# Performance work log

Hardware: AMD Instinct MI355X
Metric: run time of the kernel (lower is better)

Reference implementation:

```python
import jax, jax.numpy as jnp
import numpy as np

SCENE_BOUND = 1.5

def _trilinear_sample(vol, g):
    """torch.nn.functional.grid_sample (3D, bilinear, zeros padding, align_corners=True).

    vol: (C, D, H, W) volume.
    g:   (N, 3) normalized coords in [-1, 1], ordered (x, y, z) where
         x indexes W, y indexes H, z indexes D (torch convention).
    returns: (N, C) interpolated features.
    """
    C, D, H, W = vol.shape
    sizes = jnp.array([W, H, D], dtype=g.dtype)
    pix = (g + 1.0) * 0.5 * (sizes - 1.0)  # align_corners=True mapping
    x, y, z = pix[:, 0], pix[:, 1], pix[:, 2]
    x0f, y0f, z0f = jnp.floor(x), jnp.floor(y), jnp.floor(z)
    fx, fy, fz = x - x0f, y - y0f, z - z0f
    x0, y0, z0 = x0f.astype(jnp.int32), y0f.astype(jnp.int32), z0f.astype(jnp.int32)
    vol_flat = vol.reshape(C, -1)  # (C, D*H*W)
    out = jnp.zeros((g.shape[0], C), dtype=vol.dtype)
    for dz in (0, 1):
        for dy in (0, 1):
            for dx in (0, 1):
                xi, yi, zi = x0 + dx, y0 + dy, z0 + dz
                w = ((fx if dx else 1.0 - fx)
                     * (fy if dy else 1.0 - fy)
                     * (fz if dz else 1.0 - fz))
                inb = ((xi >= 0) & (xi < W) & (yi >= 0) & (yi < H)
                       & (zi >= 0) & (zi < D))
                xi_c = jnp.clip(xi, 0, W - 1)
                yi_c = jnp.clip(yi, 0, H - 1)
                zi_c = jnp.clip(zi, 0, D - 1)
                flat = (zi_c * H + yi_c) * W + xi_c  # (N,)
                feat = jnp.take(vol_flat, flat, axis=1)  # (C, N)
                out = out + (w * inb.astype(w.dtype))[:, None] * feat.T
    return out


def setup_inputs() -> dict:
    key = jax.random.key(0)
    k1, k2, k3, k4, k5 = jax.random.split(key, 5)
    N, R = 2_000_000, 128
    xyz = (jax.random.uniform(k1, (N, 3), dtype=jnp.float32) * 2.0 - 1.0) * (SCENE_BOUND * 0.99)
    base_density = jax.random.normal(k2, (1, 1, R, R, R), dtype=jnp.float32)
    base_sh = jax.random.normal(k3, (1, 27, R, R, R), dtype=jnp.float32)
    detail_density = jax.random.normal(k4, (1, 1, R, R, R), dtype=jnp.float32) * 0.1
    detail_sh = jax.random.normal(k5, (1, 27, R, R, R), dtype=jnp.float32) * 0.1
    return {"xyz": xyz, "base_density": base_density, "base_sh": base_sh,
            "detail_density": detail_density, "detail_sh": detail_sh}


def reference(xyz, base_density, base_sh, detail_density, detail_sh):
    # grid property: concat(base_density + detail_density, base_sh + detail_sh)
    vol = jnp.concatenate([base_density + detail_density,
                           base_sh + detail_sh], axis=1)[0]  # (C, R, R, R)
    g = xyz / SCENE_BOUND  # normalized to [-1, 1]
    return _trilinear_sample(vol, g)  # (N, C), matches query()'s permuted output
```

## Files before the change

kernel.cpp:

```cpp
#include <hip/hip_runtime.h>
#include <hip/hip_fp16.h>
#include <cstdint>
#include <cstddef>

#define RR     128
#define VV     (RR * RR * RR)
#define NCH    28
#define CPAD   32
#define NCD    16
#define NCELLS 4096
#define REG    9
#define RV     (REG * REG * REG)
#define CAPMAX 768
#define CAPMIN 576
#define OVFCAP 262144

__device__ __forceinline__ unsigned short f2h(float f) {
    __half h = __float2half(f);
    return *reinterpret_cast<unsigned short*>(&h);
}
__device__ __forceinline__ float2 up2(unsigned int u) {
    __half2 h = *reinterpret_cast<__half2*>(&u);
    return __half22float2(h);
}

__device__ __forceinline__ void point_coords(float x, float y, float z,
                                             float& px, float& py, float& pz,
                                             int& ix, int& iy, int& iz) {
    const float S = 63.5f / 1.5f;
    px = fmaf(x, S, 63.5f);
    py = fmaf(y, S, 63.5f);
    pz = fmaf(z, S, 63.5f);
    ix = min(max((int)floorf(px), 0), RR - 2);
    iy = min(max((int)floorf(py), 0), RR - 2);
    iz = min(max((int)floorf(pz), 0), RR - 2);
}

__device__ __forceinline__ void presum_body(
    int tid,
    const float* __restrict__ bden, const float* __restrict__ bsh,
    const float* __restrict__ dden, const float* __restrict__ dsh,
    unsigned short* __restrict__ ws)
{
    if (tid >= VV) return;
    unsigned short s[CPAD];
    s[0] = f2h(bden[tid] + dden[tid]);
#pragma unroll
    for (int c = 1; c < NCH; ++c) {
        size_t off = (size_t)(c - 1) * VV + tid;
        s[c] = f2h(bsh[off] + dsh[off]);
    }
#pragma unroll
    for (int c = NCH; c < CPAD; ++c) s[c] = 0;

    uint4* w = (uint4*)(ws + (size_t)tid * CPAD);
#pragma unroll
    for (int q = 0; q < 4; ++q) {
        uint4 v;
        v.x = (unsigned int)s[q*8+0] | ((unsigned int)s[q*8+1] << 16);
        v.y = (unsigned int)s[q*8+2] | ((unsigned int)s[q*8+3] << 16);
        v.z = (unsigned int)s[q*8+4] | ((unsigned int)s[q*8+5] << 16);
        v.w = (unsigned int)s[q*8+6] | ((unsigned int)s[q*8+7] << 16);
        w[q] = v;
    }
}

__global__ __launch_bounds__(256) void presum_scatter(
    const float* __restrict__ bden, const float* __restrict__ bsh,
    const float* __restrict__ dden, const float* __restrict__ dsh,
    const float* __restrict__ xyz, int N, int CAP,
    unsigned short* __restrict__ vol, float4* __restrict__ sorted,
    unsigned int* __restrict__ cur, unsigned int* __restrict__ ovf,
    unsigned int* __restrict__ ovfcnt, int presumBlocks)
{
    int b = blockIdx.x;
    if (b < presumBlocks) {
        presum_body(b * 256 + threadIdx.x, bden, bsh, dden, dsh, vol);
        return;
    }
    int n = (b - presumBlocks) * 256 + threadIdx.x;
    if (n >= N) return;
    const float* xp = xyz + (size_t)n * 3;
    float px, py, pz; int ix, iy, iz;
    point_coords(xp[0], xp[1], xp[2], px, py, pz, ix, iy, iz);
    int cell = ((iz >> 3) * NCD + (iy >> 3)) * NCD + (ix >> 3);
    unsigned int slot = atomicAdd(&cur[cell], 1u);
    if (slot < (unsigned int)CAP) {
        sorted[(size_t)cell * CAP + slot] = make_float4(px, py, pz, __int_as_float(n));
    } else {
        unsigned int o = atomicAdd(ovfcnt, 1u);
        if (o < (unsigned int)OVFCAP) ovf[o] = n;
    }
}

__global__ __launch_bounds__(512) void cell_gather(
    const unsigned short* __restrict__ vol,
    const float4* __restrict__ sorted, const unsigned int* __restrict__ cur,
    int CAP, float* __restrict__ out)
{
    __shared__ uint4 lds16[RV * 4];

    int bid = blockIdx.x;
    int cid = (bid & 7) * (NCELLS / 8) + (bid >> 3);
    int cx = cid & 15, cy = (cid >> 4) & 15, cz = cid >> 8;
    int x0 = cx << 3, y0 = cy << 3, z0 = cz << 3;

    for (int i = threadIdx.x; i < RV * 4; i += 512) {
        int v = i >> 2, j = i & 3;
        int rz = v / 81, rem = v - rz * 81;
        int ry = rem / 9, rx = rem - ry * 9;
        int zg = min(z0 + rz, RR - 1);
        int yg = min(y0 + ry, RR - 1);
        int xg = min(x0 + rx, RR - 1);
        const uint4* src = (const uint4*)(vol + (size_t)((zg * RR + yg) * RR + xg) * CPAD);
        lds16[v * 4 + (j ^ (v & 3))] = src[j];
    }
    __syncthreads();

    int cnt = (int)min(cur[cid], (unsigned int)CAP);
    const float4* sp = sorted + (size_t)cid * CAP;
    int g = threadIdx.x >> 2, t = threadIdx.x & 3;

    for (int p = g; p < cnt; p += 128) {
        float4 pt = sp[p];
        float px = pt.x, py = pt.y, pz = pt.z;
        int idx = __float_as_int(pt.w);

        float fx0 = floorf(px), fy0 = floorf(py), fz0 = floorf(pz);
        float fx = px - fx0, fy = py - fy0, fz = pz - fz0;
        int lx = min(max((int)fx0, 0), RR - 2) - x0;
        int ly = min(max((int)fy0, 0), RR - 2) - y0;
        int lz = min(max((int)fz0, 0), RR - 2) - z0;

        float wx[2] = {1.0f - fx, fx};
        float wy[2] = {1.0f - fy, fy};
        float wz[2] = {1.0f - fz, fz};

        float acc[8];
#pragma unroll
        for (int k = 0; k < 8; ++k) acc[k] = 0.0f;

#pragma unroll
        for (int dz = 0; dz < 2; ++dz)
#pragma unroll
        for (int dy = 0; dy < 2; ++dy)
#pragma unroll
        for (int dx = 0; dx < 2; ++dx) {
            int v = ((lz + dz) * 9 + (ly + dy)) * 9 + (lx + dx);
            float w = wz[dz] * wy[dy] * wx[dx];
            const uint4 q = lds16[v * 4 + (t ^ (v & 3))];
            float2 p0 = up2(q.x), p1 = up2(q.y), p2 = up2(q.z), p3 = up2(q.w);
            acc[0] = fmaf(w, p0.x, acc[0]);
            acc[1] = fmaf(w, p0.y, acc[1]);
            acc[2] = fmaf(w, p1.x, acc[2]);
            acc[3] = fmaf(w, p1.y, acc[3]);
            acc[4] = fmaf(w, p2.x, acc[4]);
            acc[5] = fmaf(w, p2.y, acc[5]);
            acc[6] = fmaf(w, p3.x, acc[6]);
            acc[7] = fmaf(w, p3.y, acc[7]);
        }

        float* op = out + (size_t)idx * NCH + t * 8;
        if (t < 3) {
            *(float4*)op       = make_float4(acc[0], acc[1], acc[2], acc[3]);
            *(float4*)(op + 4) = make_float4(acc[4], acc[5], acc[6], acc[7]);
        } else {
            *(float4*)op = make_float4(acc[0], acc[1], acc[2], acc[3]);
        }
    }
}

__global__ __launch_bounds__(256) void tail_gather(
    const float* __restrict__ xyz, const unsigned short* __restrict__ vol,
    const unsigned int* __restrict__ ovf, const unsigned int* __restrict__ ovfcnt,
    float* __restrict__ out)
{
    int m = (int)min(*ovfcnt, (unsigned int)OVFCAP);
    for (int i = blockIdx.x * 256 + threadIdx.x; i < m; i += gridDim.x * 256) {
        int n = (int)ovf[i];
        const float* xp = xyz + (size_t)n * 3;
        float px, py, pz; int ix, iy, iz;
        point_coords(xp[0], xp[1], xp[2], px, py, pz, ix, iy, iz);
        float fx = px - floorf(px), fy = py - floorf(py), fz = pz - floorf(pz);
        float wx[2] = {1.0f - fx, fx}, wy[2] = {1.0f - fy, fy}, wz[2] = {1.0f - fz, fz};
        int ibase = (iz * RR + iy) * RR + ix;
        for (int t = 0; t < 4; ++t) {
            float acc[8];
#pragma unroll
            for (int k = 0; k < 8; ++k) acc[k] = 0.0f;
#pragma unroll
            for (int dz = 0; dz < 2; ++dz)
#pragma unroll
            for (int dy = 0; dy < 2; ++dy)
#pragma unroll
            for (int dx = 0; dx < 2; ++dx) {
                int vidx = ibase + dz * (RR * RR) + dy * RR + dx;
                float w = wz[dz] * wy[dy] * wx[dx];
                const uint4 q = *(const uint4*)((const char*)vol + (size_t)vidx * (CPAD * 2) + t * 16);
                float2 p0 = up2(q.x), p1 = up2(q.y), p2 = up2(q.z), p3 = up2(q.w);
                acc[0] = fmaf(w, p0.x, acc[0]);
                acc[1] = fmaf(w, p0.y, acc[1]);
                acc[2] = fmaf(w, p1.x, acc[2]);
                acc[3] = fmaf(w, p1.y, acc[3]);
                acc[4] = fmaf(w, p2.x, acc[4]);
                acc[5] = fmaf(w, p2.y, acc[5]);
                acc[6] = fmaf(w, p3.x, acc[6]);
                acc[7] = fmaf(w, p3.y, acc[7]);
            }
            float* op = out + (size_t)n * NCH + t * 8;
            if (t < 3) {
                *(float4*)op       = make_float4(acc[0], acc[1], acc[2], acc[3]);
                *(float4*)(op + 4) = make_float4(acc[4], acc[5], acc[6], acc[7]);
            } else {
                *(float4*)op = make_float4(acc[0], acc[1], acc[2], acc[3]);
            }
        }
    }
}

__global__ __launch_bounds__(256) void presum_kernel(
    const float* __restrict__ bden, const float* __restrict__ bsh,
    const float* __restrict__ dden, const float* __restrict__ dsh,
    unsigned short* __restrict__ ws)
{
    presum_body(blockIdx.x * 256 + threadIdx.x, bden, bsh, dden, dsh, ws);
}

__global__ __launch_bounds__(256) void gather_kernel(
    const float* __restrict__ xyz,
    const unsigned short* __restrict__ vol,
    float* __restrict__ out, int N)
{
    int tid = blockIdx.x * 256 + threadIdx.x;
    int n = tid >> 2;
    int t = tid & 3;
    if (n >= N) return;

    const float* xp = xyz + (size_t)n * 3;
    float px, py, pz; int ix, iy, iz;
    point_coords(xp[0], xp[1], xp[2], px, py, pz, ix, iy, iz);
    float fx = px - floorf(px), fy = py - floorf(py), fz = pz - floorf(pz);
    float wx[2] = {1.0f - fx, fx}, wy[2] = {1.0f - fy, fy}, wz[2] = {1.0f - fz, fz};

    int ibase = (iz * RR + iy) * RR + ix;
    const char* basep = (const char*)vol + (size_t)t * 16;

    float acc[8];
#pragma unroll
    for (int k = 0; k < 8; ++k) acc[k] = 0.0f;

#pragma unroll
    for (int dz = 0; dz < 2; ++dz)
#pragma unroll
    for (int dy = 0; dy < 2; ++dy)
#pragma unroll
    for (int dx = 0; dx < 2; ++dx) {
        int vidx = ibase + dz * (RR * RR) + dy * RR + dx;
        float w = wz[dz] * wy[dy] * wx[dx];
        const uint4 q = *(const uint4*)(basep + (size_t)vidx * (CPAD * 2));
        float2 p0 = up2(q.x), p1 = up2(q.y), p2 = up2(q.z), p3 = up2(q.w);
        acc[0] = fmaf(w, p0.x, acc[0]);
        acc[1] = fmaf(w, p0.y, acc[1]);
        acc[2] = fmaf(w, p1.x, acc[2]);
        acc[3] = fmaf(w, p1.y, acc[3]);
        acc[4] = fmaf(w, p2.x, acc[4]);
        acc[5] = fmaf(w, p2.y, acc[5]);
        acc[6] = fmaf(w, p3.x, acc[6]);
        acc[7] = fmaf(w, p3.y, acc[7]);
    }

    float* op = out + (size_t)n * NCH + t * 8;
    if (t < 3) {
        *(float4*)op       = make_float4(acc[0], acc[1], acc[2], acc[3]);
        *(float4*)(op + 4) = make_float4(acc[4], acc[5], acc[6], acc[7]);
    } else {
        *(float4*)op = make_float4(acc[0], acc[1], acc[2], acc[3]);
    }
}

__global__ __launch_bounds__(256) void gather_fallback(
    const float* __restrict__ xyz,
    const float* __restrict__ bden, const float* __restrict__ bsh,
    const float* __restrict__ dden, const float* __restrict__ dsh,
    float* __restrict__ out, int N)
{
    int n = blockIdx.x * 256 + threadIdx.x;
    if (n >= N) return;
    const float* xp = xyz + (size_t)n * 3;
    float px, py, pz; int ix, iy, iz;
    point_coords(xp[0], xp[1], xp[2], px, py, pz, ix, iy, iz);
    float fx = px - floorf(px), fy = py - floorf(py), fz = pz - floorf(pz);
    float wx[2] = {1.0f - fx, fx}, wy[2] = {1.0f - fy, fy}, wz[2] = {1.0f - fz, fz};

    int idx[8]; float w[8];
#pragma unroll
    for (int k = 0; k < 8; ++k) {
        int dz = (k >> 2) & 1, dy = (k >> 1) & 1, dx = k & 1;
        idx[k] = ((iz + dz) * RR + (iy + dy)) * RR + (ix + dx);
        w[k] = wz[dz] * wy[dy] * wx[dx];
    }
#pragma unroll
    for (int c = 0; c < NCH; ++c) {
        const float* bp = (c == 0) ? bden : (bsh + (size_t)(c - 1) * VV);
        const float* dp = (c == 0) ? dden : (dsh + (size_t)(c - 1) * VV);
        float a = 0.0f;
#pragma unroll
        for (int k = 0; k < 8; ++k)
            a = fmaf(w[k], bp[idx[k]] + dp[idx[k]], a);
        out[(size_t)n * NCH + c] = a;
    }
}

extern "C" void kernel_launch(void* const* d_in, const int* in_sizes, int n_in,
                              void* d_out, int out_size, void* d_ws, size_t ws_size,
                              hipStream_t stream) {
    const float* xyz  = (const float*)d_in[0];
    const float* bden = (const float*)d_in[1];
    const float* bsh  = (const float*)d_in[2];
    const float* dden = (const float*)d_in[3];
    const float* dsh  = (const float*)d_in[4];
    float* out = (float*)d_out;
    int N = in_sizes[0] / 3;

    size_t volBytes = (size_t)VV * CPAD * sizeof(unsigned short);
    size_t ovfBytes = (size_t)OVFCAP * 4;
    size_t ctrBytes = (size_t)(NCELLS + 1) * 4;

    long long availForSorted = (long long)ws_size - (long long)(volBytes + ovfBytes + ctrBytes + 64);
    int CAP = 0;
    if (availForSorted > 0) {
        long long c = availForSorted / ((long long)NCELLS * 16);
        CAP = (int)(c > CAPMAX ? CAPMAX : c);
    }

    if (CAP >= CAPMIN) {
        char* w = (char*)d_ws;
        float4* sorted      = (float4*)w;
        size_t sortedBytes  = (size_t)NCELLS * CAP * 16;
        unsigned short* vol = (unsigned short*)(w + sortedBytes);
        unsigned int* ovf   = (unsigned int*)(w + sortedBytes + volBytes);
        unsigned int* cur   = (unsigned int*)(w + sortedBytes + volBytes + ovfBytes);
        unsigned int* ovfcnt = cur + NCELLS;

        hipMemsetAsync(cur, 0, (NCELLS + 1) * sizeof(unsigned int), stream);
        int presumBlocks  = (VV + 255) / 256;
        int scatterBlocks = (N + 255) / 256;
        presum_scatter<<<presumBlocks + scatterBlocks, 256, 0, stream>>>(
            bden, bsh, dden, dsh, xyz, N, CAP,
            vol, sorted, cur, ovf, ovfcnt, presumBlocks);
        cell_gather<<<NCELLS, 512, 0, stream>>>(vol, sorted, cur, CAP, out);
        tail_gather<<<32, 256, 0, stream>>>(xyz, vol, ovf, ovfcnt, out);
    } else if (ws_size >= volBytes) {
        presum_kernel<<<(VV + 255) / 256, 256, 0, stream>>>(
            bden, bsh, dden, dsh, (unsigned short*)d_ws);
        long long threads = (long long)N * 4;
        gather_kernel<<<(unsigned int)((threads + 255) / 256), 256, 0, stream>>>(
            xyz, (const unsigned short*)d_ws, out, N);
    } else {
        gather_fallback<<<(N + 255) / 256, 256, 0, stream>>>(
            xyz, bden, bsh, dden, dsh, out, N);
    }
}
```

Baseline: 799.3 us.

## Shard cell counters into sub-buckets, chunk volume layout, fuse tail gather

Spreads the scatter atomics over 8 sub-buckets per cell, chosen by block index, so fewer threads contend on the same counter. The gather block merges the sub-buckets through a small prefix sum. The packed fp16 volume is rearranged into 64-voxel chunks so the presum writes and the halo loads coalesce. The overflow tail pass is folded into extra blocks of the cell gather kernel, capacities are sized from the mean occupancy, and presum loads are batched with a higher occupancy launch bound. Costs are more bucket memory and a per-point sub-bucket lookup.

```diff
diff --git a/kernel.cpp b/kernel.cpp
--- a/kernel.cpp
+++ b/kernel.cpp
@@ -2,6 +2,7 @@
 #include <hip/hip_fp16.h>
 #include <cstdint>
 #include <cstddef>
+#include <cmath>
 
 #define RR     128
 #define VV     (RR * RR * RR)
@@ -9,11 +10,11 @@
 #define CPAD   32
 #define NCD    16
 #define NCELLS 4096
+#define NSUB   8
 #define REG    9
 #define RV     (REG * REG * REG)
-#define CAPMAX 768
-#define CAPMIN 576
-#define OVFCAP 262144
+#define OVFCAP (1 << 20)
+#define TAILB  32
 
 __device__ __forceinline__ unsigned short f2h(float f) {
     __half h = __float2half(f);
@@ -22,6 +23,10 @@
 __device__ __forceinline__ float2 up2(unsigned int u) {
     __half2 h = *reinterpret_cast<__half2*>(&u);
     return __half22float2(h);
+}
+
+__device__ __forceinline__ size_t chunk_at(int V, int q) {
+    return ((size_t)(V >> 6)) * 256 + (q << 6) + (V & 63);
 }
 
 __device__ __forceinline__ void point_coords(float x, float y, float z,
@@ -36,24 +41,43 @@
     iz = min(max((int)floorf(pz), 0), RR - 2);
 }
 
+__device__ __forceinline__ void corner_accum(
+    const uint4 q, float w, float* acc)
+{
+    float2 p0 = up2(q.x), p1 = up2(q.y), p2 = up2(q.z), p3 = up2(q.w);
+    acc[0] = fmaf(w, p0.x, acc[0]);
+    acc[1] = fmaf(w, p0.y, acc[1]);
+    acc[2] = fmaf(w, p1.x, acc[2]);
+    acc[3] = fmaf(w, p1.y, acc[3]);
+    acc[4] = fmaf(w, p2.x, acc[4]);
+    acc[5] = fmaf(w, p2.y, acc[5]);
+    acc[6] = fmaf(w, p3.x, acc[6]);
+    acc[7] = fmaf(w, p3.y, acc[7]);
+}
+
 __device__ __forceinline__ void presum_body(
     int tid,
     const float* __restrict__ bden, const float* __restrict__ bsh,
     const float* __restrict__ dden, const float* __restrict__ dsh,
-    unsigned short* __restrict__ ws)
+    unsigned short* __restrict__ vol)
 {
     if (tid >= VV) return;
+    float vb[27], vd[27];
+    float v0 = bden[tid] + dden[tid];
+#pragma unroll
+    for (int c = 0; c < 27; ++c) vb[c] = bsh[(size_t)c * VV + tid];
+#pragma unroll
+    for (int c = 0; c < 27; ++c) vd[c] = dsh[(size_t)c * VV + tid];
+
     unsigned short s[CPAD];
-    s[0] = f2h(bden[tid] + dden[tid]);
-#pragma unroll
-    for (int c = 1; c < NCH; ++c) {
-        size_t off = (size_t)(c - 1) * VV + tid;
-        s[c] = f2h(bsh[off] + dsh[off]);
-    }
+    s[0] = f2h(v0);
+#pragma unroll
+    for (int c = 0; c < 27; ++c) s[c + 1] = f2h(vb[c] + vd[c]);
 #pragma unroll
     for (int c = NCH; c < CPAD; ++c) s[c] = 0;
 
-    uint4* w = (uint4*)(ws + (size_t)tid * CPAD);
+    uint4* volq = (uint4*)vol;
+    int grp = tid >> 6, lane = tid & 63;
 #pragma unroll
     for (int q = 0; q < 4; ++q) {
         uint4 v;
@@ -61,14 +85,14 @@
         v.y = (unsigned int)s[q*8+2] | ((unsigned int)s[q*8+3] << 16);
         v.z = (unsigned int)s[q*8+4] | ((unsigned int)s[q*8+5] << 16);
         v.w = (unsigned int)s[q*8+6] | ((unsigned int)s[q*8+7] << 16);
-        w[q] = v;
-    }
-}
-
-__global__ __launch_bounds__(256) void presum_scatter(
+        volq[(size_t)grp * 256 + (q << 6) + lane] = v;
+    }
+}
+
+__global__ __launch_bounds__(256, 4) void presum_scatter(
     const float* __restrict__ bden, const float* __restrict__ bsh,
     const float* __restrict__ dden, const float* __restrict__ dsh,
-    const float* __restrict__ xyz, int N, int CAP,
+    const float* __restrict__ xyz, int N, int CAPS,
     unsigned short* __restrict__ vol, float4* __restrict__ sorted,
     unsigned int* __restrict__ cur, unsigned int* __restrict__ ovf,
     unsigned int* __restrict__ ovfcnt, int presumBlocks)
@@ -84,9 +108,11 @@
     float px, py, pz; int ix, iy, iz;
     point_coords(xp[0], xp[1], xp[2], px, py, pz, ix, iy, iz);
     int cell = ((iz >> 3) * NCD + (iy >> 3)) * NCD + (ix >> 3);
-    unsigned int slot = atomicAdd(&cur[cell], 1u);
-    if (slot < (unsigned int)CAP) {
-        sorted[(size_t)cell * CAP + slot] = make_float4(px, py, pz, __int_as_float(n));
+    int sub = b & 7;
+    unsigned int slot = atomicAdd(&cur[sub * NCELLS + cell], 1u);
+    if (slot < (unsigned int)CAPS) {
+        sorted[((size_t)sub * NCELLS + cell) * CAPS + slot] =
+            make_float4(px, py, pz, __int_as_float(n));
     } else {
         unsigned int o = atomicAdd(ovfcnt, 1u);
         if (o < (unsigned int)OVFCAP) ovf[o] = n;
@@ -94,35 +120,89 @@
 }
 
 __global__ __launch_bounds__(512) void cell_gather(
-    const unsigned short* __restrict__ vol,
+    const unsigned short* __restrict__ vol, const float* __restrict__ xyz,
     const float4* __restrict__ sorted, const unsigned int* __restrict__ cur,
-    int CAP, float* __restrict__ out)
-{
+    const unsigned int* __restrict__ ovf, const unsigned int* __restrict__ ovfcnt,
+    int CAPS, float* __restrict__ out)
+{
+    const uint4* vol4 = (const uint4*)vol;
+    int bid = blockIdx.x;
+
+    if (bid >= NCELLS) {
+        int m = (int)min(*ovfcnt, (unsigned int)OVFCAP);
+        for (int i = (bid - NCELLS) * 512 + threadIdx.x; i < m; i += TAILB * 512) {
+            int n = (int)ovf[i];
+            const float* xp = xyz + (size_t)n * 3;
+            float px, py, pz; int ix, iy, iz;
+            point_coords(xp[0], xp[1], xp[2], px, py, pz, ix, iy, iz);
+            float fx = px - floorf(px), fy = py - floorf(py), fz = pz - floorf(pz);
+            float wx[2] = {1.0f - fx, fx}, wy[2] = {1.0f - fy, fy}, wz[2] = {1.0f - fz, fz};
+            int ibase = (iz * RR + iy) * RR + ix;
+            for (int t = 0; t < 4; ++t) {
+                float acc[8];
+#pragma unroll
+                for (int k = 0; k < 8; ++k) acc[k] = 0.0f;
+#pragma unroll
+                for (int dz = 0; dz < 2; ++dz)
+#pragma unroll
+                for (int dy = 0; dy < 2; ++dy)
+#pragma unroll
+                for (int dx = 0; dx < 2; ++dx) {
+                    int vidx = ibase + dz * (RR * RR) + dy * RR + dx;
+                    float w = wz[dz] * wy[dy] * wx[dx];
+                    corner_accum(vol4[chunk_at(vidx, t)], w, acc);
+                }
+                float* op = out + (size_t)n * NCH + t * 8;
+                if (t < 3) {
+                    *(float4*)op       = make_float4(acc[0], acc[1], acc[2], acc[3]);
+                    *(float4*)(op + 4) = make_float4(acc[4], acc[5], acc[6], acc[7]);
+                } else {
+                    *(float4*)op = make_float4(acc[0], acc[1], acc[2], acc[3]);
+                }
+            }
+        }
+        return;
+    }
+
     __shared__ uint4 lds16[RV * 4];
-
-    int bid = blockIdx.x;
+    __shared__ unsigned int pref[NSUB + 1];
+
     int cid = (bid & 7) * (NCELLS / 8) + (bid >> 3);
     int cx = cid & 15, cy = (cid >> 4) & 15, cz = cid >> 8;
     int x0 = cx << 3, y0 = cy << 3, z0 = cz << 3;
 
-    for (int i = threadIdx.x; i < RV * 4; i += 512) {
-        int v = i >> 2, j = i & 3;
+    if (threadIdx.x == 0) {
+        unsigned int a = 0;
+        pref[0] = 0;
+#pragma unroll
+        for (int s = 0; s < NSUB; ++s) {
+            a += min(cur[s * NCELLS + cid], (unsigned int)CAPS);
+            pref[s + 1] = a;
+        }
+    }
+
+    for (int i = threadIdx.x; i < 4 * RV; i += 512) {
+        int q = i / RV;
+        int v = i - q * RV;
         int rz = v / 81, rem = v - rz * 81;
         int ry = rem / 9, rx = rem - ry * 9;
         int zg = min(z0 + rz, RR - 1);
         int yg = min(y0 + ry, RR - 1);
         int xg = min(x0 + rx, RR - 1);
-        const uint4* src = (const uint4*)(vol + (size_t)((zg * RR + yg) * RR + xg) * CPAD);
-        lds16[v * 4 + (j ^ (v & 3))] = src[j];
+        int V = (zg * RR + yg) * RR + xg;
+        lds16[v * 4 + (q ^ (v & 3))] = vol4[chunk_at(V, q)];
     }
     __syncthreads();
 
-    int cnt = (int)min(cur[cid], (unsigned int)CAP);
-    const float4* sp = sorted + (size_t)cid * CAP;
+    int total = (int)pref[NSUB];
     int g = threadIdx.x >> 2, t = threadIdx.x & 3;
 
-    for (int p = g; p < cnt; p += 128) {
-        float4 pt = sp[p];
+    for (int vp = g; vp < total; vp += 128) {
+        int s = 0;
+#pragma unroll
+        for (int k = 0; k < NSUB - 1; ++k) s += (vp >= (int)pref[k + 1]);
+        int p = vp - (int)pref[s];
+        float4 pt = sorted[((size_t)s * NCELLS + cid) * CAPS + p];
         float px = pt.x, py = pt.y, pz = pt.z;
         int idx = __float_as_int(pt.w);
 
@@ -148,16 +228,7 @@
         for (int dx = 0; dx < 2; ++dx) {
             int v = ((lz + dz) * 9 + (ly + dy)) * 9 + (lx + dx);
             float w = wz[dz] * wy[dy] * wx[dx];
-            const uint4 q = lds16[v * 4 + (t ^ (v & 3))];
-            float2 p0 = up2(q.x), p1 = up2(q.y), p2 = up2(q.z), p3 = up2(q.w);
-            acc[0] = fmaf(w, p0.x, acc[0]);
-            acc[1] = fmaf(w, p0.y, acc[1]);
-            acc[2] = fmaf(w, p1.x, acc[2]);
-            acc[3] = fmaf(w, p1.y, acc[3]);
-            acc[4] = fmaf(w, p2.x, acc[4]);
-            acc[5] = fmaf(w, p2.y, acc[5]);
-            acc[6] = fmaf(w, p3.x, acc[6]);
-            acc[7] = fmaf(w, p3.y, acc[7]);
+            corner_accum(lds16[v * 4 + (t ^ (v & 3))], w, acc);
         }
 
         float* op = out + (size_t)idx * NCH + t * 8;
@@ -170,60 +241,12 @@
     }
 }
 
-__global__ __launch_bounds__(256) void tail_gather(
-    const float* __restrict__ xyz, const unsigned short* __restrict__ vol,
-    const unsigned int* __restrict__ ovf, const unsigned int* __restrict__ ovfcnt,
-    float* __restrict__ out)
-{
-    int m = (int)min(*ovfcnt, (unsigned int)OVFCAP);
-    for (int i = blockIdx.x * 256 + threadIdx.x; i < m; i += gridDim.x * 256) {
-        int n = (int)ovf[i];
-        const float* xp = xyz + (size_t)n * 3;
-        float px, py, pz; int ix, iy, iz;
-        point_coords(xp[0], xp[1], xp[2], px, py, pz, ix, iy, iz);
-        float fx = px - floorf(px), fy = py - floorf(py), fz = pz - floorf(pz);
-        float wx[2] = {1.0f - fx, fx}, wy[2] = {1.0f - fy, fy}, wz[2] = {1.0f - fz, fz};
-        int ibase = (iz * RR + iy) * RR + ix;
-        for (int t = 0; t < 4; ++t) {
-            float acc[8];
-#pragma unroll
-            for (int k = 0; k < 8; ++k) acc[k] = 0.0f;
-#pragma unroll
-            for (int dz = 0; dz < 2; ++dz)
-#pragma unroll
-            for (int dy = 0; dy < 2; ++dy)
-#pragma unroll
-            for (int dx = 0; dx < 2; ++dx) {
-                int vidx = ibase + dz * (RR * RR) + dy * RR + dx;
-                float w = wz[dz] * wy[dy] * wx[dx];
-                const uint4 q = *(const uint4*)((const char*)vol + (size_t)vidx * (CPAD * 2) + t * 16);
-                float2 p0 = up2(q.x), p1 = up2(q.y), p2 = up2(q.z), p3 = up2(q.w);
-                acc[0] = fmaf(w, p0.x, acc[0]);
-                acc[1] = fmaf(w, p0.y, acc[1]);
-                acc[2] = fmaf(w, p1.x, acc[2]);
-                acc[3] = fmaf(w, p1.y, acc[3]);
-                acc[4] = fmaf(w, p2.x, acc[4]);
-                acc[5] = fmaf(w, p2.y, acc[5]);
-                acc[6] = fmaf(w, p3.x, acc[6]);
-                acc[7] = fmaf(w, p3.y, acc[7]);
-            }
-            float* op = out + (size_t)n * NCH + t * 8;
-            if (t < 3) {
-                *(float4*)op       = make_float4(acc[0], acc[1], acc[2], acc[3]);
-                *(float4*)(op + 4) = make_float4(acc[4], acc[5], acc[6], acc[7]);
-            } else {
-                *(float4*)op = make_float4(acc[0], acc[1], acc[2], acc[3]);
-            }
-        }
-    }
-}
-
-__global__ __launch_bounds__(256) void presum_kernel(
+__global__ __launch_bounds__(256, 4) void presum_kernel(
     const float* __restrict__ bden, const float* __restrict__ bsh,
     const float* __restrict__ dden, const float* __restrict__ dsh,
-    unsigned short* __restrict__ ws)
-{
-    presum_body(blockIdx.x * 256 + threadIdx.x, bden, bsh, dden, dsh, ws);
+    unsigned short* __restrict__ vol)
+{
+    presum_body(blockIdx.x * 256 + threadIdx.x, bden, bsh, dden, dsh, vol);
 }
 
 __global__ __launch_bounds__(256) void gather_kernel(
@@ -235,6 +258,7 @@
     int n = tid >> 2;
     int t = tid & 3;
     if (n >= N) return;
+    const uint4* vol4 = (const uint4*)vol;
 
     const float* xp = xyz + (size_t)n * 3;
     float px, py, pz; int ix, iy, iz;
@@ -243,7 +267,6 @@
     float wx[2] = {1.0f - fx, fx}, wy[2] = {1.0f - fy, fy}, wz[2] = {1.0f - fz, fz};
 
     int ibase = (iz * RR + iy) * RR + ix;
-    const char* basep = (const char*)vol + (size_t)t * 16;
 
     float acc[8];
 #pragma unroll
@@ -257,16 +280,7 @@
     for (int dx = 0; dx < 2; ++dx) {
         int vidx = ibase + dz * (RR * RR) + dy * RR + dx;
         float w = wz[dz] * wy[dy] * wx[dx];
-        const uint4 q = *(const uint4*)(basep + (size_t)vidx * (CPAD * 2));
-        float2 p0 = up2(q.x), p1 = up2(q.y), p2 = up2(q.z), p3 = up2(q.w);
-        acc[0] = fmaf(w, p0.x, acc[0]);
-        acc[1] = fmaf(w, p0.y, acc[1]);
-        acc[2] = fmaf(w, p1.x, acc[2]);
-        acc[3] = fmaf(w, p1.y, acc[3]);
-        acc[4] = fmaf(w, p2.x, acc[4]);
-        acc[5] = fmaf(w, p2.y, acc[5]);
-        acc[6] = fmaf(w, p3.x, acc[6]);
-        acc[7] = fmaf(w, p3.y, acc[7]);
+        corner_accum(vol4[chunk_at(vidx, t)], w, acc);
     }
 
     float* op = out + (size_t)n * NCH + t * 8;
@@ -321,37 +335,44 @@
     const float* dsh  = (const float*)d_in[4];
     float* out = (float*)d_out;
     int N = in_sizes[0] / 3;
+    if (N <= 0) return;
 
     size_t volBytes = (size_t)VV * CPAD * sizeof(unsigned short);
     size_t ovfBytes = (size_t)OVFCAP * 4;
-    size_t ctrBytes = (size_t)(NCELLS + 1) * 4;
-
-    long long availForSorted = (long long)ws_size - (long long)(volBytes + ovfBytes + ctrBytes + 64);
-    int CAP = 0;
-    if (availForSorted > 0) {
-        long long c = availForSorted / ((long long)NCELLS * 16);
-        CAP = (int)(c > CAPMAX ? CAPMAX : c);
-    }
-
-    if (CAP >= CAPMIN) {
+    size_t ctrBytes = (size_t)(NSUB * NCELLS + 1) * 4;
+
+    int nb = NSUB * NCELLS;
+    int mean = (N + nb - 1) / nb;
+    double sg = sqrt((double)mean);
+    int target  = mean + (int)(5.0 * sg) + 8;
+    int capsMin = mean + (int)(1.5 * sg) + 2;
+
+    long long avail = (long long)ws_size - (long long)(volBytes + ovfBytes + ctrBytes + 64);
+    int CAPS = 0;
+    if (avail > 0) {
+        long long c = avail / ((long long)nb * 16);
+        CAPS = (int)(c > target ? target : c);
+    }
+
+    if (CAPS >= capsMin) {
         char* w = (char*)d_ws;
         float4* sorted      = (float4*)w;
-        size_t sortedBytes  = (size_t)NCELLS * CAP * 16;
+        size_t sortedBytes  = (size_t)nb * CAPS * 16;
         unsigned short* vol = (unsigned short*)(w + sortedBytes);
         unsigned int* ovf   = (unsigned int*)(w + sortedBytes + volBytes);
         unsigned int* cur   = (unsigned int*)(w + sortedBytes + volBytes + ovfBytes);
-        unsigned int* ovfcnt = cur + NCELLS;
-
-        hipMemsetAsync(cur, 0, (NCELLS + 1) * sizeof(unsigned int), stream);
-        int presumBlocks  = (VV + 255) / 256;
+        unsigned int* ovfcnt = cur + NSUB * NCELLS;
+
+        hipMemsetAsync(cur, 0, ctrBytes, stream);
+        int presumBlocks  = VV / 256;
         int scatterBlocks = (N + 255) / 256;
         presum_scatter<<<presumBlocks + scatterBlocks, 256, 0, stream>>>(
-            bden, bsh, dden, dsh, xyz, N, CAP,
+            bden, bsh, dden, dsh, xyz, N, CAPS,
             vol, sorted, cur, ovf, ovfcnt, presumBlocks);
-        cell_gather<<<NCELLS, 512, 0, stream>>>(vol, sorted, cur, CAP, out);
-        tail_gather<<<32, 256, 0, stream>>>(xyz, vol, ovf, ovfcnt, out);
+        cell_gather<<<NCELLS + TAILB, 512, 0, stream>>>(
+            vol, xyz, sorted, cur, ovf, ovfcnt, CAPS, out);
     } else if (ws_size >= volBytes) {
-        presum_kernel<<<(VV + 255) / 256, 256, 0, stream>>>(
+        presum_kernel<<<VV / 256, 256, 0, stream>>>(
             bden, bsh, dden, dsh, (unsigned short*)d_ws);
         long long threads = (long long)N * 4;
         gather_kernel<<<(unsigned int)((threads + 255) / 256), 256, 0, stream>>>(
```

Result: faster. 749.0 us (-6.3%).
